# Kernel tuning notes

Hardware: AMD Instinct MI355X
Metric: run time of the kernel (lower is better)

Reference implementation:

```python
import jax, jax.numpy as jnp
import numpy as np

B, E, DIM = 8, 2048, 512
KERNEL = 8
DECAY_CONSTANT = 1.0


def _forward(x, weight, bias, decay_value):
    # x: (B, E, S) with S == dim; weight: (K, S); bias: (S,); decay_value: (2, 1)
    K, dim = weight.shape
    Bb, Ee, S = x.shape
    i = jnp.arange(dim)[:, None]
    j = jnp.arange(dim)[None, :]
    # decayed upper-triangular weight: W[k, i, j] = weight[k, j] * dv^((j-i)/c) for j >= i
    dv = jnp.clip(decay_value[1, 0], 0.9, 1.0)
    d = dv ** ((j - i).astype(x.dtype) / DECAY_CONSTANT)  # (S, S)
    W = jnp.where(j >= i, weight[:, None, :] * d[None], jnp.zeros((), x.dtype))  # (K, S, S)
    p = K - 1
    padded = jnp.pad(x, ((0, 0), (p, p), (0, 0)))  # zero-pad sequence axis
    # shifted stack: stacked[b, k, e] = x[b, e + k - (K-1)] (zeros out of range) -> causal taps
    stacked = jnp.stack([padded[:, k:Ee + k] for k in range(K)], axis=1)  # (B, K, E, S)
    out = jnp.einsum('bkei,kij->bej', stacked, W) + bias
    return out


def setup_inputs() -> dict:
    key = jax.random.key(0)
    k1, k2 = jax.random.split(key)
    x = jax.random.normal(k1, (B, E, DIM), dtype=jnp.float32)
    weight = jax.random.normal(k2, (KERNEL, DIM), dtype=jnp.float32)
    bias = jnp.zeros((DIM,), dtype=jnp.float32)
    decay_value = jnp.ones((2, 1), dtype=jnp.float32)
    return {"x": x, "weight": weight, "bias": bias, "decay_value": decay_value}


def reference(x, weight, bias, decay_value):
    return _forward(x, weight, bias, decay_value)
```

## Files before the change

kernel.cpp:

```cpp
#include <hip/hip_runtime.h>


#define B_    8
#define E_    2048
#define DIM_  512
#define K_    8
#define TILE_E 25
#define NROWS  (TILE_E + K_ - 1)

__global__ __launch_bounds__(256) void krl_fused(
    const float* __restrict__ x,
    const float* __restrict__ weight,
    const float* __restrict__ bias,
    const float* __restrict__ decay,
    float* __restrict__ out)
{
    __shared__ float yls[NROWS][DIM_];

    const int tile = blockIdx.x;
    const int b    = blockIdx.y;
    const int e0   = tile * TILE_E;
    const int nout = min(TILE_E, E_ - e0);
    const int nscan = nout + K_ - 1;

    const int t    = threadIdx.x;
    const int lane = t & 63;
    const int wave = t >> 6;

    float dv = decay[1];
    dv = fminf(fmaxf(dv, 0.9f), 1.0f);
    const float dv2 = dv * dv;
    const float dv4 = dv2 * dv2;
    const float dv8 = dv4 * dv4;

    for (int r = wave; r < nscan; r += 4) {
        const int eg = e0 - (K_ - 1) + r;
        float tl[8];
        if (eg >= 0) {
            const float4* xp = (const float4*)(x + ((size_t)b * E_ + eg) * DIM_ + lane * 8);
            const float4 a0 = xp[0];
            const float4 a1 = xp[1];
            const float xv[8] = {a0.x, a0.y, a0.z, a0.w, a1.x, a1.y, a1.z, a1.w};
            tl[0] = xv[0];
            #pragma unroll
            for (int m = 1; m < 8; ++m) tl[m] = fmaf(dv, tl[m - 1], xv[m]);
            float v  = tl[7];
            float ap = dv8;
            #pragma unroll
            for (int off = 1; off < 64; off <<= 1) {
                float up = __shfl_up(v, off, 64);
                if (lane >= off) v = fmaf(ap, up, v);
                ap *= ap;
            }
            float carry = __shfl_up(v, 1, 64);
            if (lane == 0) carry = 0.f;
            float dp = dv;
            #pragma unroll
            for (int m = 0; m < 8; ++m) { tl[m] = fmaf(dp, carry, tl[m]); dp *= dv; }
        } else {
            #pragma unroll
            for (int m = 0; m < 8; ++m) tl[m] = 0.f;
        }
        float4* yp = (float4*)(&yls[r][lane * 8]);
        yp[0] = make_float4(tl[0], tl[1], tl[2], tl[3]);
        yp[1] = make_float4(tl[4], tl[5], tl[6], tl[7]);
    }
    __syncthreads();

    const int g  = t >> 7;
    const int jf = (t & 127) * 4;

    float4 w[K_];
    #pragma unroll
    for (int k = 0; k < K_; ++k) w[k] = *(const float4*)(weight + k * DIM_ + jf);
    const float4 bi = *(const float4*)(bias + jf);

    for (int te = g; te < nout; te += 2) {
        float4 acc = bi;
        #pragma unroll
        for (int k = 0; k < K_; ++k) {
            const float4 yv = *(const float4*)(&yls[te + k][jf]);
            acc.x = fmaf(w[k].x, yv.x, acc.x);
            acc.y = fmaf(w[k].y, yv.y, acc.y);
            acc.z = fmaf(w[k].z, yv.z, acc.z);
            acc.w = fmaf(w[k].w, yv.w, acc.w);
        }
        *(float4*)(out + ((size_t)b * E_ + e0 + te) * DIM_ + jf) = acc;
    }
}

extern "C" void kernel_launch(void* const* d_in, const int* in_sizes, int n_in,
                              void* d_out, int out_size, void* d_ws, size_t ws_size,
                              hipStream_t stream) {
    const float* x      = (const float*)d_in[0];
    const float* weight = (const float*)d_in[1];
    const float* bias   = (const float*)d_in[2];
    const float* decay  = (const float*)d_in[3];
    float* out = (float*)d_out;

    dim3 grid((E_ + TILE_E - 1) / TILE_E, B_);
    dim3 block(256);
    krl_fused<<<grid, block, 0, stream>>>(x, weight, bias, decay, out);
}
```

Baseline: 93.39 us.

## Split fused scan+conv kernel into separate scan and conv kernels via workspace

Replaces the fused tile kernel, which recomputed the decayed scan for K-1 halo rows per tile in shared memory, with two kernels. The first writes the per-row scan to a global workspace once. The second computes the 8-tap causal convolution by reading shifted rows from that workspace. This removes the halo recompute and the shared-memory occupancy limit, at the cost of an extra 32 MB round trip through global memory and a second launch.

```diff
diff --git a/kernel.cpp b/kernel.cpp
--- a/kernel.cpp
+++ b/kernel.cpp
@@ -5,27 +5,16 @@
 #define E_    2048
 #define DIM_  512
 #define K_    8
-#define TILE_E 25
-#define NROWS  (TILE_E + K_ - 1)
 
-__global__ __launch_bounds__(256) void krl_fused(
+__global__ __launch_bounds__(256) void krl_scan(
     const float* __restrict__ x,
-    const float* __restrict__ weight,
-    const float* __restrict__ bias,
     const float* __restrict__ decay,
-    float* __restrict__ out)
+    float* __restrict__ y)
 {
-    __shared__ float yls[NROWS][DIM_];
-
-    const int tile = blockIdx.x;
-    const int b    = blockIdx.y;
-    const int e0   = tile * TILE_E;
-    const int nout = min(TILE_E, E_ - e0);
-    const int nscan = nout + K_ - 1;
-
     const int t    = threadIdx.x;
     const int lane = t & 63;
     const int wave = t >> 6;
+    const int row  = blockIdx.x * 4 + wave;
 
     float dv = decay[1];
     dv = fminf(fmaxf(dv, 0.9f), 1.0f);
@@ -33,60 +22,62 @@
     const float dv4 = dv2 * dv2;
     const float dv8 = dv4 * dv4;
 
-    for (int r = wave; r < nscan; r += 4) {
-        const int eg = e0 - (K_ - 1) + r;
-        float tl[8];
+    const float4* xp = (const float4*)(x + (size_t)row * DIM_ + lane * 8);
+    const float4 a0 = xp[0];
+    const float4 a1 = xp[1];
+    const float xv[8] = {a0.x, a0.y, a0.z, a0.w, a1.x, a1.y, a1.z, a1.w};
+
+    float tl[8];
+    tl[0] = xv[0];
+    #pragma unroll
+    for (int m = 1; m < 8; ++m) tl[m] = fmaf(dv, tl[m - 1], xv[m]);
+
+    float v  = tl[7];
+    float ap = dv8;
+    #pragma unroll
+    for (int off = 1; off < 64; off <<= 1) {
+        float up = __shfl_up(v, off, 64);
+        if (lane >= off) v = fmaf(ap, up, v);
+        ap *= ap;
+    }
+    float carry = __shfl_up(v, 1, 64);
+    if (lane == 0) carry = 0.f;
+    float dp = dv;
+    #pragma unroll
+    for (int m = 0; m < 8; ++m) { tl[m] = fmaf(dp, carry, tl[m]); dp *= dv; }
+
+    float4* yp = (float4*)(y + (size_t)row * DIM_ + lane * 8);
+    yp[0] = make_float4(tl[0], tl[1], tl[2], tl[3]);
+    yp[1] = make_float4(tl[4], tl[5], tl[6], tl[7]);
+}
+
+__global__ __launch_bounds__(256) void krl_conv(
+    const float* __restrict__ y,
+    const float* __restrict__ weight,
+    const float* __restrict__ bias,
+    float* __restrict__ out)
+{
+    const int gid   = blockIdx.x * 256 + threadIdx.x;
+    const int chunk = gid & 127;
+    const int e     = (gid >> 7) & (E_ - 1);
+    const int b     = gid >> 18;
+    const int jf    = chunk * 4;
+
+    float4 acc = *(const float4*)(bias + jf);
+
+    #pragma unroll
+    for (int k = 0; k < K_; ++k) {
+        const int eg = e + k - (K_ - 1);
         if (eg >= 0) {
-            const float4* xp = (const float4*)(x + ((size_t)b * E_ + eg) * DIM_ + lane * 8);
-            const float4 a0 = xp[0];
-            const float4 a1 = xp[1];
-            const float xv[8] = {a0.x, a0.y, a0.z, a0.w, a1.x, a1.y, a1.z, a1.w};
-            tl[0] = xv[0];
-            #pragma unroll
-            for (int m = 1; m < 8; ++m) tl[m] = fmaf(dv, tl[m - 1], xv[m]);
-            float v  = tl[7];
-            float ap = dv8;
-            #pragma unroll
-            for (int off = 1; off < 64; off <<= 1) {
-                float up = __shfl_up(v, off, 64);
-                if (lane >= off) v = fmaf(ap, up, v);
-                ap *= ap;
-            }
-            float carry = __shfl_up(v, 1, 64);
-            if (lane == 0) carry = 0.f;
-            float dp = dv;
-            #pragma unroll
-            for (int m = 0; m < 8; ++m) { tl[m] = fmaf(dp, carry, tl[m]); dp *= dv; }
-        } else {
-            #pragma unroll
-            for (int m = 0; m < 8; ++m) tl[m] = 0.f;
+            const float4 w  = *(const float4*)(weight + k * DIM_ + jf);
+            const float4 yv = *(const float4*)(y + ((size_t)b * E_ + eg) * DIM_ + jf);
+            acc.x = fmaf(w.x, yv.x, acc.x);
+            acc.y = fmaf(w.y, yv.y, acc.y);
+            acc.z = fmaf(w.z, yv.z, acc.z);
+            acc.w = fmaf(w.w, yv.w, acc.w);
         }
-        float4* yp = (float4*)(&yls[r][lane * 8]);
-        yp[0] = make_float4(tl[0], tl[1], tl[2], tl[3]);
-        yp[1] = make_float4(tl[4], tl[5], tl[6], tl[7]);
     }
-    __syncthreads();
-
-    const int g  = t >> 7;
-    const int jf = (t & 127) * 4;
-
-    float4 w[K_];
-    #pragma unroll
-    for (int k = 0; k < K_; ++k) w[k] = *(const float4*)(weight + k * DIM_ + jf);
-    const float4 bi = *(const float4*)(bias + jf);
-
-    for (int te = g; te < nout; te += 2) {
-        float4 acc = bi;
-        #pragma unroll
-        for (int k = 0; k < K_; ++k) {
-            const float4 yv = *(const float4*)(&yls[te + k][jf]);
-            acc.x = fmaf(w[k].x, yv.x, acc.x);
-            acc.y = fmaf(w[k].y, yv.y, acc.y);
-            acc.z = fmaf(w[k].z, yv.z, acc.z);
-            acc.w = fmaf(w[k].w, yv.w, acc.w);
-        }
-        *(float4*)(out + ((size_t)b * E_ + e0 + te) * DIM_ + jf) = acc;
-    }
+    *(float4*)(out + ((size_t)b * E_ + e) * DIM_ + jf) = acc;
 }
 
 extern "C" void kernel_launch(void* const* d_in, const int* in_sizes, int n_in,
@@ -97,8 +88,8 @@
     const float* bias   = (const float*)d_in[2];
     const float* decay  = (const float*)d_in[3];
     float* out = (float*)d_out;
+    float* y   = (float*)d_ws;
 
-    dim3 grid((E_ + TILE_E - 1) / TILE_E, B_);
-    dim3 block(256);
-    krl_fused<<<grid, block, 0, stream>>>(x, weight, bias, decay, out);
+    krl_scan<<<dim3((B_ * E_) / 4), dim3(256), 0, stream>>>(x, decay, y);
+    krl_conv<<<dim3((B_ * E_ * (DIM_ / 4)) / 256), dim3(256), 0, stream>>>(y, weight, bias, out);
 }
```

New measurement: 116.5 us. 24.8% more time.
